# Kernel optimization log

Hardware: AMD Instinct MI355X
Metric: run time of the kernel (lower is better)

The kernel has to match this reference:

```python
import jax, jax.numpy as jnp
import numpy as np


def setup_inputs() -> dict:
    key = jax.random.key(0)
    ks = jax.random.split(key, 6)
    B, S, D_IN, D_OUT, E, R = 4, 2048, 4096, 4096, 8, 16
    x = jax.random.normal(ks[0], (B, S, D_IN), dtype=jnp.float32)
    probs = jax.random.uniform(ks[1], (B, E), dtype=jnp.float32)
    router_probs = probs / jnp.sum(probs, axis=-1, keepdims=True)
    weight = jax.random.normal(ks[2], (D_OUT, D_IN), dtype=jnp.float32) * 0.02
    bias = jax.random.normal(ks[3], (D_OUT,), dtype=jnp.float32) * 0.02
    lora_A = jax.random.normal(ks[4], (E, R, D_IN), dtype=jnp.float32) * 0.02
    lora_B = jax.random.normal(ks[5], (E, D_OUT, R), dtype=jnp.float32) * 0.02
    return {"x": x, "router_probs": router_probs, "weight": weight,
            "bias": bias, "lora_A": lora_A, "lora_B": lora_B}


def reference(x, router_probs, weight, bias, lora_A, lora_B):
    scaling = 2.0
    # base linear: [b,s,i] @ [o,i]^T + bias
    base_out = jnp.einsum('bsi,oi->bso', x, weight) + bias
    # low-rank per-expert projection: [b,s,e,r] (small: r=16)
    mid = jnp.einsum('bsi,eri->bser', x, lora_A)
    # weight by router probs (per batch, per expert) before up-projection
    mid_w = mid * router_probs[:, None, :, None]
    # sum over experts fused into the up-projection contraction
    delta = jnp.einsum('bser,eor->bso', mid_w, lora_B) * scaling
    return base_out + delta
```

## Files before the change

kernel.cpp:

```cpp
#include <hip/hip_runtime.h>


typedef _Float16 half8 __attribute__((ext_vector_type(8)));
typedef _Float16 half4 __attribute__((ext_vector_type(4)));
typedef float    f32x4 __attribute__((ext_vector_type(4)));

#define M_TOT 8192
#define N_TOT 4096
#define K_IN  4096
#define KA    4224
#define NT    132

__device__ __forceinline__ void cvt_store4(_Float16* p, float4 f) {
  half4 h;
  h[0] = (_Float16)f.x; h[1] = (_Float16)f.y;
  h[2] = (_Float16)f.z; h[3] = (_Float16)f.w;
  *(half4*)p = h;
}

template <int LOG2C, int DCOLS>
__global__ __launch_bounds__(256) void convert_f32_f16_t(
    const float* __restrict__ src, _Float16* __restrict__ dst, int total8) {
  for (int i = blockIdx.x * 256 + threadIdx.x; i < total8;
       i += gridDim.x * 256) {
    int base = i << 3;
    int r = base >> LOG2C;
    int c = base & ((1 << LOG2C) - 1);
    const float4* s = (const float4*)(src + (size_t)base);
    float4 f0 = s[0], f1 = s[1];
    half8 h;
    h[0]=(_Float16)f0.x; h[1]=(_Float16)f0.y; h[2]=(_Float16)f0.z; h[3]=(_Float16)f0.w;
    h[4]=(_Float16)f1.x; h[5]=(_Float16)f1.y; h[6]=(_Float16)f1.z; h[7]=(_Float16)f1.w;
    *(half8*)(dst + (size_t)r * DCOLS + c) = h;
  }
}

__global__ __launch_bounds__(256) void wtail_gather_f16(
    const float* __restrict__ loraB, _Float16* __restrict__ Wa) {
  int idx = blockIdx.x * 256 + threadIdx.x;
  int n = idx >> 7, j = idx & 127;
  int e = j >> 4, r = j & 15;
  Wa[(size_t)n * KA + K_IN + j] =
      (_Float16)loraB[((size_t)e * N_TOT + n) * 16 + r];
}

__global__ __launch_bounds__(256) void lorabf_gather_f32(
    const float* __restrict__ loraB, float* __restrict__ lorabf) {
  int idx = blockIdx.x * 256 + threadIdx.x;
  int n = idx >> 7, j = idx & 127;
  int e = j >> 4, r = j & 15;
  lorabf[(size_t)n * 128 + j] = loraB[((size_t)e * N_TOT + n) * 16 + r];
}

__global__ __launch_bounds__(256) void mid2_kernel(
    _Float16* __restrict__ Xa, const _Float16* __restrict__ lAh,
    const float* __restrict__ router) {
  __shared__ _Float16 As[32 * 64];
  __shared__ _Float16 Bs[128 * 64];
  int tid = threadIdx.x, lane = tid & 63, w = tid >> 6;
  int m0 = blockIdx.x * 32;
  int b = m0 >> 11;
  f32x4 acc[2][2] = {};

  int scol = ((lane & 7) ^ (lane >> 3)) * 16;
  int ln15 = lane & 15, ln4 = lane >> 4;

  for (int ks = 0; ks < 64; ++ks) {
    int kb = ks * 128;
    {
      const char* s = (const char*)Xa +
          (size_t)(m0 + w * 8 + (lane >> 3)) * (KA * 2) + kb + scol;
      __builtin_amdgcn_global_load_lds(
          (const __attribute__((address_space(1))) void*)s,
          (__attribute__((address_space(3))) void*)((char*)As + w * 1024 + lane * 16), 16, 0, 0);
    }
#pragma unroll
    for (int i = 0; i < 4; ++i) {
      const char* s = (const char*)lAh +
          (size_t)((w * 4 + i) * 8 + (lane >> 3)) * (4096 * 2) + kb + scol;
      __builtin_amdgcn_global_load_lds(
          (const __attribute__((address_space(1))) void*)s,
          (__attribute__((address_space(3))) void*)((char*)Bs + (w * 4 + i) * 1024 + lane * 16), 16, 0, 0);
    }
    __syncthreads();
#pragma unroll
    for (int kk = 0; kk < 2; ++kk) {
      int rs = (((kk * 4 + ln4) ^ (ln15 & 7)) << 4);
      half8 a[2], bf[2];
#pragma unroll
      for (int mi = 0; mi < 2; ++mi)
        a[mi] = *(const half8*)((const char*)As + (mi * 16 + ln15) * 128 + rs);
#pragma unroll
      for (int ni = 0; ni < 2; ++ni)
        bf[ni] = *(const half8*)((const char*)Bs + (w * 32 + ni * 16 + ln15) * 128 + rs);
#pragma unroll
      for (int mi = 0; mi < 2; ++mi)
#pragma unroll
        for (int ni = 0; ni < 2; ++ni)
          acc[mi][ni] = __builtin_amdgcn_mfma_f32_16x16x32_f16(a[mi], bf[ni], acc[mi][ni], 0, 0, 0);
    }
    __syncthreads();
  }

#pragma unroll
  for (int ni = 0; ni < 2; ++ni) {
    int j = w * 32 + ni * 16 + ln15;
    int e = j >> 4;
    float sc = 2.0f * router[b * 8 + e];
#pragma unroll
    for (int mi = 0; mi < 2; ++mi) {
      f32x4 v = acc[mi][ni];
#pragma unroll
      for (int jj = 0; jj < 4; ++jj) {
        int m = m0 + mi * 16 + ln4 * 4 + jj;
        Xa[(size_t)m * KA + K_IN + j] = (_Float16)(v[jj] * sc);
      }
    }
  }
}

__global__ __launch_bounds__(256) void mid_kernel(
    const float* __restrict__ x, const float* __restrict__ loraA,
    const float* __restrict__ router, float* __restrict__ midw) {
  __shared__ _Float16 As[32 * 64];
  __shared__ _Float16 Bs[128 * 64];
  int tid = threadIdx.x, lane = tid & 63, w = tid >> 6;
  int m0 = blockIdx.x * 32;
  int b = m0 >> 11;
  f32x4 acc[2][2] = {};
  for (int ks = 0; ks < 64; ++ks) {
    int k0 = ks * 64;
#pragma unroll
    for (int it = 0; it < 2; ++it) {
      int idx = tid + it * 256;
      int r = idx >> 4, c4 = idx & 15;
      float4 f = *(const float4*)(x + (size_t)(m0 + r) * K_IN + k0 + c4 * 4);
      cvt_store4(As + r * 64 + c4 * 4, f);
    }
#pragma unroll
    for (int it = 0; it < 8; ++it) {
      int idx = tid + it * 256;
      int r = idx >> 4, c4 = idx & 15;
      float4 f = *(const float4*)(loraA + (size_t)r * K_IN + k0 + c4 * 4);
      cvt_store4(Bs + r * 64 + c4 * 4, f);
    }
    __syncthreads();
#pragma unroll
    for (int kk = 0; kk < 2; ++kk) {
      half8 a[2], bf[2];
#pragma unroll
      for (int mi = 0; mi < 2; ++mi)
        a[mi] = *(const half8*)(As + (mi * 16 + (lane & 15)) * 64 + kk * 32 + (lane >> 4) * 8);
#pragma unroll
      for (int ni = 0; ni < 2; ++ni)
        bf[ni] = *(const half8*)(Bs + (w * 32 + ni * 16 + (lane & 15)) * 64 + kk * 32 + (lane >> 4) * 8);
#pragma unroll
      for (int mi = 0; mi < 2; ++mi)
#pragma unroll
        for (int ni = 0; ni < 2; ++ni)
          acc[mi][ni] = __builtin_amdgcn_mfma_f32_16x16x32_f16(a[mi], bf[ni], acc[mi][ni], 0, 0, 0);
    }
    __syncthreads();
  }
#pragma unroll
  for (int ni = 0; ni < 2; ++ni) {
    int j = w * 32 + ni * 16 + (lane & 15);
    int e = j >> 4;
    float sc = 2.0f * router[b * 8 + e];
#pragma unroll
    for (int mi = 0; mi < 2; ++mi) {
      f32x4 v = acc[mi][ni];
#pragma unroll
      for (int jj = 0; jj < 4; ++jj) {
        int m = m0 + mi * 16 + (lane >> 4) * 4 + jj;
        midw[(size_t)m * 128 + j] = v[jj] * sc;
      }
    }
  }
}

#define BAR    __builtin_amdgcn_s_barrier()
#define SCHED0 __builtin_amdgcn_sched_barrier(0)
#define VMW8   asm volatile("s_waitcnt vmcnt(8)" ::: "memory")
#define VMW4   asm volatile("s_waitcnt vmcnt(4)" ::: "memory")
#define VMW0   asm volatile("s_waitcnt vmcnt(0)" ::: "memory")
#define GLOAD(src, dst) __builtin_amdgcn_global_load_lds( \
    (const __attribute__((address_space(1))) void*)(src), \
    (__attribute__((address_space(3))) void*)(dst), 16, 0, 0)

#define READS(SL) do { \
  _Pragma("unroll") for (int ni = 0; ni < 4; ++ni) \
    bF[ni] = *(const half8*)(LDS + 65536 + (SL) * 16384 + \
                             (wn + ni * 16 + ln15) * 64 + rslot); \
  _Pragma("unroll") for (int mi = 0; mi < 8; ++mi) \
    aF[mi] = *(const half8*)(LDS + (SL) * 16384 + \
                             (wm + mi * 16 + ln15) * 64 + rslot); \
  } while (0)

#define STAGE4(TT, SL) do { \
  const char* sA_ = XpC + (size_t)(TT) * 64; \
  const char* sB_ = WpC + (size_t)(TT) * 64; \
  GLOAD(sA_ + goff0, LDS + (SL) * 16384 + l0); \
  GLOAD(sA_ + goff1, LDS + (SL) * 16384 + l1); \
  GLOAD(sB_ + goff0, LDS + 65536 + (SL) * 16384 + l0); \
  GLOAD(sB_ + goff1, LDS + 65536 + (SL) * 16384 + l1); \
  } while (0)

#define MFMA32 do { \
  _Pragma("unroll") for (int mi = 0; mi < 8; ++mi) \
    _Pragma("unroll") for (int ni = 0; ni < 4; ++ni) \
      acc[mi][ni] = __builtin_amdgcn_mfma_f32_16x16x32_f16( \
          aF[mi], bF[ni], acc[mi][ni], 0, 0, 0); \
  } while (0)

#define TILE_FULL(SL) do { \
  READS(SL); \
  STAGE4(t4 + (SL) + 3, ((SL) + 3) & 3); \
  MFMA32; VMW8; BAR; SCHED0; \
  } while (0)

__global__ __launch_bounds__(512, 2) void gemm256(
    const _Float16* __restrict__ Xa, const _Float16* __restrict__ Wa,
    const float* __restrict__ bias, float* __restrict__ out) {
  __shared__ __align__(16) char LDS[131072];

  int tid = threadIdx.x, lane = tid & 63, w = tid >> 6;
  int ln15 = lane & 15, ln4 = lane >> 4;
  int wm = (w >> 2) * 128, wn = (w & 3) * 64;

  int bid = blockIdx.x;
  int xcd = bid & 7, idx = bid >> 3;
  int mt = (xcd & 3) * 8 + (idx & 7);
  int nt = (xcd >> 2) * 8 + (idx >> 3);
  int m0 = mt << 8, n0 = nt << 8;

  const char* XpC = (const char*)Xa + (size_t)m0 * (KA * 2);
  const char* WpC = (const char*)Wa + (size_t)n0 * (KA * 2);

  int i0 = tid, i1 = tid + 512;
  int goff0 = (i0 >> 2) * (KA * 2) + (((i0 & 3) ^ ((i0 >> 3) & 3)) * 16);
  int goff1 = (i1 >> 2) * (KA * 2) + (((i1 & 3) ^ ((i1 >> 3) & 3)) * 16);
  int l0 = i0 * 16, l1 = i1 * 16;

  int rslot = ((ln4 ^ ((lane >> 1) & 3)) * 16);

  f32x4 acc[8][4] = {};
  half8 aF[8], bF[4];

  STAGE4(0, 0); STAGE4(1, 1); STAGE4(2, 2);
  VMW8; BAR; SCHED0;

#pragma unroll 1
  for (int t4 = 0; t4 < NT - 4; t4 += 4) {
    TILE_FULL(0); TILE_FULL(1); TILE_FULL(2); TILE_FULL(3);
  }

  { READS(0); STAGE4(131, 3); MFMA32; VMW8; BAR; SCHED0; }
  { READS(1); MFMA32; VMW4; BAR; SCHED0; }
  { READS(2); MFMA32; VMW0; BAR; SCHED0; }
  { READS(3); MFMA32; }

#pragma unroll
  for (int ni = 0; ni < 4; ++ni) {
    int n = n0 + wn + ni * 16 + ln15;
    float bz = bias[n];
#pragma unroll
    for (int mi = 0; mi < 8; ++mi) {
      f32x4 v = acc[mi][ni];
      int mb = m0 + wm + mi * 16 + ln4 * 4;
#pragma unroll
      for (int jj = 0; jj < 4; ++jj)
        out[(size_t)(mb + jj) * N_TOT + n] = v[jj] + bz;
    }
  }
}

__global__ __launch_bounds__(256) void gemm_fallback(
    const float* __restrict__ x, const float* __restrict__ wgt,
    const float* __restrict__ midw, const float* __restrict__ lorabf,
    const float* __restrict__ bias, float* __restrict__ out) {
  __shared__ _Float16 As[128 * 64];
  __shared__ _Float16 Bs[128 * 64];
  int tid = threadIdx.x, lane = tid & 63, w = tid >> 6;
  int mt = blockIdx.x & 63, nt = blockIdx.x >> 6;
  int m0 = mt << 7, n0 = nt << 7;
  int wm = (w >> 1) * 64, wn = (w & 1) * 64;
  f32x4 acc[4][4] = {};
  for (int ks = 0; ks < 66; ++ks) {
    int k0 = ks * 64;
    const float *asrc, *bsrc; size_t astr, bstr; int ac, bc;
    if (ks < 64) { asrc = x;    astr = K_IN; ac = k0;        bsrc = wgt;    bstr = K_IN; bc = k0; }
    else         { asrc = midw; astr = 128;  ac = k0 - K_IN; bsrc = lorabf; bstr = 128;  bc = k0 - K_IN; }
#pragma unroll
    for (int it = 0; it < 8; ++it) {
      int idx = tid + it * 256;
      int r = idx >> 4, c4 = idx & 15;
      float4 fa = *(const float4*)(asrc + (size_t)(m0 + r) * astr + ac + c4 * 4);
      cvt_store4(As + r * 64 + c4 * 4, fa);
      float4 fb = *(const float4*)(bsrc + (size_t)(n0 + r) * bstr + bc + c4 * 4);
      cvt_store4(Bs + r * 64 + c4 * 4, fb);
    }
    __syncthreads();
#pragma unroll
    for (int kk = 0; kk < 2; ++kk) {
      half8 a[4], bf[4];
#pragma unroll
      for (int mi = 0; mi < 4; ++mi)
        a[mi] = *(const half8*)(As + (wm + mi * 16 + (lane & 15)) * 64 + kk * 32 + (lane >> 4) * 8);
#pragma unroll
      for (int ni = 0; ni < 4; ++ni)
        bf[ni] = *(const half8*)(Bs + (wn + ni * 16 + (lane & 15)) * 64 + kk * 32 + (lane >> 4) * 8);
#pragma unroll
      for (int mi = 0; mi < 4; ++mi)
#pragma unroll
        for (int ni = 0; ni < 4; ++ni)
          acc[mi][ni] = __builtin_amdgcn_mfma_f32_16x16x32_f16(a[mi], bf[ni], acc[mi][ni], 0, 0, 0);
    }
    __syncthreads();
  }
#pragma unroll
  for (int ni = 0; ni < 4; ++ni) {
    int n = n0 + wn + ni * 16 + (lane & 15);
    float bz = bias[n];
#pragma unroll
    for (int mi = 0; mi < 4; ++mi) {
      f32x4 v = acc[mi][ni];
      int mbase = m0 + wm + mi * 16 + (lane >> 4) * 4;
#pragma unroll
      for (int jj = 0; jj < 4; ++jj)
        out[(size_t)(mbase + jj) * N_TOT + n] = v[jj] + bz;
    }
  }
}

extern "C" void kernel_launch(void* const* d_in, const int* in_sizes, int n_in,
                              void* d_out, int out_size, void* d_ws, size_t ws_size,
                              hipStream_t stream) {
  const float* x      = (const float*)d_in[0];
  const float* router = (const float*)d_in[1];
  const float* wgt    = (const float*)d_in[2];
  const float* bias   = (const float*)d_in[3];
  const float* loraA  = (const float*)d_in[4];
  const float* loraB  = (const float*)d_in[5];
  float* out = (float*)d_out;
  char* ws = (char*)d_ws;

  const size_t XAUG_B = (size_t)M_TOT * KA * 2;
  const size_t WAUG_B = (size_t)N_TOT * KA * 2;
  const size_t LAH_B  = (size_t)128 * K_IN * 2;
  const size_t MIDW_B = (size_t)M_TOT * 128 * 4;
  bool fast = ws_size >= XAUG_B + WAUG_B + LAH_B;

  if (fast) {
    _Float16* Xa  = (_Float16*)ws;
    _Float16* Wa  = (_Float16*)(ws + XAUG_B);
    _Float16* lAh = (_Float16*)(ws + XAUG_B + WAUG_B);
    convert_f32_f16_t<12, KA><<<2048, 256, 0, stream>>>(x,   Xa, M_TOT * K_IN / 8);
    convert_f32_f16_t<12, KA><<<2048, 256, 0, stream>>>(wgt, Wa, N_TOT * K_IN / 8);
    convert_f32_f16_t<12, 4096><<<256, 256, 0, stream>>>(loraA, lAh, 128 * K_IN / 8);
    wtail_gather_f16<<<2048, 256, 0, stream>>>(loraB, Wa);
    mid2_kernel<<<256, 256, 0, stream>>>(Xa, lAh, router);
    gemm256<<<512, 512, 0, stream>>>(Xa, Wa, bias, out);
  } else {
    float* midw   = (float*)ws;
    float* lorabf = (float*)(ws + MIDW_B);
    lorabf_gather_f32<<<2048, 256, 0, stream>>>(loraB, lorabf);
    mid_kernel<<<256, 256, 0, stream>>>(x, loraA, router, midw);
    gemm_fallback<<<2048, 256, 0, stream>>>(x, wgt, midw, lorabf, bias, out);
  }
}
```

Measured before the change: 364.8 us.

## Switch main GEMM to 32x32 MFMA and split-K the LoRA down-projection

The main GEMM switches from 16x16x32 to 32x32x16 MFMA tiles. The shared-memory layout changes so each 64-lane fragment is read contiguously, replacing the XOR swizzle. The LoRA mid projection moves from a 256-block serial-K kernel to a 2048-block split-K kernel that reads fp32 x directly and accumulates with atomics into a zeroed fp32 buffer. A separate pass then scales by the router and packs into the augmented X. This adds extra launches, atomics and a reread of x in fp32 in exchange for more parallelism and a different GEMM inner loop.

Measured after the change: 472.3 us. 1.29x slower.

```diff
diff --git a/kernel.cpp b/kernel.cpp
--- a/kernel.cpp
+++ b/kernel.cpp
@@ -3,7 +3,8 @@
 
 typedef _Float16 half8 __attribute__((ext_vector_type(8)));
 typedef _Float16 half4 __attribute__((ext_vector_type(4)));
-typedef float    f32x4 __attribute__((ext_vector_type(4)));
+typedef float    f32x4  __attribute__((ext_vector_type(4)));
+typedef float    f32x16 __attribute__((ext_vector_type(16)));
 
 #define M_TOT 8192
 #define N_TOT 4096
@@ -52,6 +53,78 @@
   lorabf[(size_t)n * 128 + j] = loraB[((size_t)e * N_TOT + n) * 16 + r];
 }
 
+__global__ __launch_bounds__(256) void zero_f4(float4* p, int n) {
+  int i = blockIdx.x * 256 + threadIdx.x;
+  if (i < n) { float4 z = {0.f, 0.f, 0.f, 0.f}; p[i] = z; }
+}
+
+__global__ __launch_bounds__(256) void midk_kernel(
+    const float* __restrict__ x, const float* __restrict__ loraA,
+    float* __restrict__ midw) {
+  __shared__ _Float16 As[32 * 64];
+  __shared__ _Float16 Bs[128 * 64];
+  int tid = threadIdx.x, lane = tid & 63, w = tid >> 6;
+  int m0 = (blockIdx.x >> 3) * 32;
+  int ks0 = (blockIdx.x & 7) * 8;
+  f32x4 acc[2][2] = {};
+  for (int ks = ks0; ks < ks0 + 8; ++ks) {
+    int k0 = ks * 64;
+#pragma unroll
+    for (int it = 0; it < 2; ++it) {
+      int idx = tid + it * 256;
+      int r = idx >> 4, c4 = idx & 15;
+      float4 f = *(const float4*)(x + (size_t)(m0 + r) * K_IN + k0 + c4 * 4);
+      cvt_store4(As + r * 64 + c4 * 4, f);
+    }
+#pragma unroll
+    for (int it = 0; it < 8; ++it) {
+      int idx = tid + it * 256;
+      int r = idx >> 4, c4 = idx & 15;
+      float4 f = *(const float4*)(loraA + (size_t)r * K_IN + k0 + c4 * 4);
+      cvt_store4(Bs + r * 64 + c4 * 4, f);
+    }
+    __syncthreads();
+#pragma unroll
+    for (int kk = 0; kk < 2; ++kk) {
+      half8 a[2], bf[2];
+#pragma unroll
+      for (int mi = 0; mi < 2; ++mi)
+        a[mi] = *(const half8*)(As + (mi * 16 + (lane & 15)) * 64 + kk * 32 + (lane >> 4) * 8);
+#pragma unroll
+      for (int ni = 0; ni < 2; ++ni)
+        bf[ni] = *(const half8*)(Bs + (w * 32 + ni * 16 + (lane & 15)) * 64 + kk * 32 + (lane >> 4) * 8);
+#pragma unroll
+      for (int mi = 0; mi < 2; ++mi)
+#pragma unroll
+        for (int ni = 0; ni < 2; ++ni)
+          acc[mi][ni] = __builtin_amdgcn_mfma_f32_16x16x32_f16(a[mi], bf[ni], acc[mi][ni], 0, 0, 0);
+    }
+    __syncthreads();
+  }
+#pragma unroll
+  for (int ni = 0; ni < 2; ++ni) {
+    int j = w * 32 + ni * 16 + (lane & 15);
+#pragma unroll
+    for (int mi = 0; mi < 2; ++mi) {
+      f32x4 v = acc[mi][ni];
+#pragma unroll
+      for (int jj = 0; jj < 4; ++jj) {
+        int m = m0 + mi * 16 + (lane >> 4) * 4 + jj;
+        atomicAdd(&midw[(size_t)m * 128 + j], v[jj]);
+      }
+    }
+  }
+}
+
+__global__ __launch_bounds__(256) void scale_pack(
+    const float* __restrict__ midw, const float* __restrict__ router,
+    _Float16* __restrict__ Xa) {
+  int idx = blockIdx.x * 256 + threadIdx.x;
+  int m = idx >> 7, j = idx & 127;
+  int b = m >> 11, e = j >> 4;
+  Xa[(size_t)m * KA + K_IN + j] = (_Float16)(2.0f * router[b * 8 + e] * midw[idx]);
+}
+
 __global__ __launch_bounds__(256) void mid2_kernel(
     _Float16* __restrict__ Xa, const _Float16* __restrict__ lAh,
     const float* __restrict__ router) {
@@ -61,10 +134,8 @@
   int m0 = blockIdx.x * 32;
   int b = m0 >> 11;
   f32x4 acc[2][2] = {};
-
   int scol = ((lane & 7) ^ (lane >> 3)) * 16;
   int ln15 = lane & 15, ln4 = lane >> 4;
-
   for (int ks = 0; ks < 64; ++ks) {
     int kb = ks * 128;
     {
@@ -101,7 +172,6 @@
     }
     __syncthreads();
   }
-
 #pragma unroll
   for (int ni = 0; ni < 2; ++ni) {
     int j = w * 32 + ni * 16 + ln15;
@@ -189,34 +259,37 @@
     (__attribute__((address_space(3))) void*)(dst), 16, 0, 0)
 
 #define READS(SL) do { \
-  _Pragma("unroll") for (int ni = 0; ni < 4; ++ni) \
-    bF[ni] = *(const half8*)(LDS + 65536 + (SL) * 16384 + \
-                             (wn + ni * 16 + ln15) * 64 + rslot); \
-  _Pragma("unroll") for (int mi = 0; mi < 8; ++mi) \
-    aF[mi] = *(const half8*)(LDS + (SL) * 16384 + \
-                             (wm + mi * 16 + ln15) * 64 + rslot); \
+  _Pragma("unroll") for (int ni = 0; ni < 2; ++ni) \
+    _Pragma("unroll") for (int kk = 0; kk < 2; ++kk) \
+      bF[ni][kk] = *(const half8*)(LDS + 65536 + (SL) * 16384 + \
+                                   (((nbB + ni) * 2 + kk) << 10) + lane * 16); \
+  _Pragma("unroll") for (int mi = 0; mi < 4; ++mi) \
+    _Pragma("unroll") for (int kk = 0; kk < 2; ++kk) \
+      aF[mi][kk] = *(const half8*)(LDS + (SL) * 16384 + \
+                                   (((mbB + mi) * 2 + kk) << 10) + lane * 16); \
   } while (0)
 
 #define STAGE4(TT, SL) do { \
   const char* sA_ = XpC + (size_t)(TT) * 64; \
   const char* sB_ = WpC + (size_t)(TT) * 64; \
-  GLOAD(sA_ + goff0, LDS + (SL) * 16384 + l0); \
-  GLOAD(sA_ + goff1, LDS + (SL) * 16384 + l1); \
-  GLOAD(sB_ + goff0, LDS + 65536 + (SL) * 16384 + l0); \
-  GLOAD(sB_ + goff1, LDS + 65536 + (SL) * 16384 + l1); \
+  GLOAD(sA_ + goffA[0], LDS + (SL) * 16384 + lof[0]); \
+  GLOAD(sA_ + goffA[1], LDS + (SL) * 16384 + lof[1]); \
+  GLOAD(sB_ + goffA[0], LDS + 65536 + (SL) * 16384 + lof[0]); \
+  GLOAD(sB_ + goffA[1], LDS + 65536 + (SL) * 16384 + lof[1]); \
   } while (0)
 
-#define MFMA32 do { \
-  _Pragma("unroll") for (int mi = 0; mi < 8; ++mi) \
-    _Pragma("unroll") for (int ni = 0; ni < 4; ++ni) \
-      acc[mi][ni] = __builtin_amdgcn_mfma_f32_16x16x32_f16( \
-          aF[mi], bF[ni], acc[mi][ni], 0, 0, 0); \
+#define MFMA16X do { \
+  _Pragma("unroll") for (int mi = 0; mi < 4; ++mi) \
+    _Pragma("unroll") for (int ni = 0; ni < 2; ++ni) \
+      _Pragma("unroll") for (int kk = 0; kk < 2; ++kk) \
+        acc[mi][ni] = __builtin_amdgcn_mfma_f32_32x32x16_f16( \
+            aF[mi][kk], bF[ni][kk], acc[mi][ni], 0, 0, 0); \
   } while (0)
 
 #define TILE_FULL(SL) do { \
   READS(SL); \
   STAGE4(t4 + (SL) + 3, ((SL) + 3) & 3); \
-  MFMA32; VMW8; BAR; SCHED0; \
+  MFMA16X; VMW8; BAR; SCHED0; \
   } while (0)
 
 __global__ __launch_bounds__(512, 2) void gemm256(
@@ -225,8 +298,8 @@
   __shared__ __align__(16) char LDS[131072];
 
   int tid = threadIdx.x, lane = tid & 63, w = tid >> 6;
-  int ln15 = lane & 15, ln4 = lane >> 4;
-  int wm = (w >> 2) * 128, wn = (w & 3) * 64;
+  int mbB = (w >> 2) * 4;
+  int nbB = (w & 3) * 2;
 
   int bid = blockIdx.x;
   int xcd = bid & 7, idx = bid >> 3;
@@ -237,15 +310,19 @@
   const char* XpC = (const char*)Xa + (size_t)m0 * (KA * 2);
   const char* WpC = (const char*)Wa + (size_t)n0 * (KA * 2);
 
-  int i0 = tid, i1 = tid + 512;
-  int goff0 = (i0 >> 2) * (KA * 2) + (((i0 & 3) ^ ((i0 >> 3) & 3)) * 16);
-  int goff1 = (i1 >> 2) * (KA * 2) + (((i1 & 3) ^ ((i1 >> 3) & 3)) * 16);
-  int l0 = i0 * 16, l1 = i1 * 16;
-
-  int rslot = ((ln4 ^ ((lane >> 1) & 3)) * 16);
-
-  f32x4 acc[8][4] = {};
-  half8 aF[8], bF[4];
+  int goffA[2], lof[2];
+#pragma unroll
+  for (int j = 0; j < 2; ++j) {
+    int ix = j * 512 + tid;
+    int c = ix >> 6, lp = ix & 63;
+    int row = (c >> 1) * 32 + (lp & 31);
+    int kb = ((c & 1) << 5) + ((lp >> 5) << 4);
+    goffA[j] = row * (KA * 2) + kb;
+    lof[j] = ix * 16;
+  }
+
+  f32x16 acc[4][2] = {};
+  half8 aF[4][2], bF[2][2];
 
   STAGE4(0, 0); STAGE4(1, 1); STAGE4(2, 2);
   VMW8; BAR; SCHED0;
@@ -255,22 +332,24 @@
     TILE_FULL(0); TILE_FULL(1); TILE_FULL(2); TILE_FULL(3);
   }
 
-  { READS(0); STAGE4(131, 3); MFMA32; VMW8; BAR; SCHED0; }
-  { READS(1); MFMA32; VMW4; BAR; SCHED0; }
-  { READS(2); MFMA32; VMW0; BAR; SCHED0; }
-  { READS(3); MFMA32; }
-
-#pragma unroll
-  for (int ni = 0; ni < 4; ++ni) {
-    int n = n0 + wn + ni * 16 + ln15;
+  { READS(0); STAGE4(131, 3); MFMA16X; VMW8; BAR; SCHED0; }
+  { READS(1); MFMA16X; VMW4; BAR; SCHED0; }
+  { READS(2); MFMA16X; VMW0; BAR; SCHED0; }
+  { READS(3); MFMA16X; }
+
+#pragma unroll
+  for (int ni = 0; ni < 2; ++ni) {
+    int n = n0 + (nbB + ni) * 32 + (lane & 31);
     float bz = bias[n];
 #pragma unroll
-    for (int mi = 0; mi < 8; ++mi) {
-      f32x4 v = acc[mi][ni];
-      int mb = m0 + wm + mi * 16 + ln4 * 4;
-#pragma unroll
-      for (int jj = 0; jj < 4; ++jj)
-        out[(size_t)(mb + jj) * N_TOT + n] = v[jj] + bz;
+    for (int mi = 0; mi < 4; ++mi) {
+      f32x16 v = acc[mi][ni];
+      int rb = m0 + (mbB + mi) * 32 + ((lane >> 5) << 2);
+#pragma unroll
+      for (int reg = 0; reg < 16; ++reg) {
+        int r = rb + (reg & 3) + ((reg >> 2) << 3);
+        out[(size_t)r * N_TOT + n] = v[reg] + bz;
+      }
     }
   }
 }
@@ -349,9 +428,20 @@
   const size_t WAUG_B = (size_t)N_TOT * KA * 2;
   const size_t LAH_B  = (size_t)128 * K_IN * 2;
   const size_t MIDW_B = (size_t)M_TOT * 128 * 4;
-  bool fast = ws_size >= XAUG_B + WAUG_B + LAH_B;
-
-  if (fast) {
+  const size_t MIDF_B = MIDW_B;
+
+  if (ws_size >= XAUG_B + WAUG_B + MIDW_B) {
+    _Float16* Xa  = (_Float16*)ws;
+    _Float16* Wa  = (_Float16*)(ws + XAUG_B);
+    float* midw   = (float*)(ws + XAUG_B + WAUG_B);
+    convert_f32_f16_t<12, KA><<<2048, 256, 0, stream>>>(x,   Xa, M_TOT * K_IN / 8);
+    convert_f32_f16_t<12, KA><<<2048, 256, 0, stream>>>(wgt, Wa, N_TOT * K_IN / 8);
+    wtail_gather_f16<<<2048, 256, 0, stream>>>(loraB, Wa);
+    zero_f4<<<1024, 256, 0, stream>>>((float4*)midw, M_TOT * 128 / 4);
+    midk_kernel<<<2048, 256, 0, stream>>>(x, loraA, midw);
+    scale_pack<<<4096, 256, 0, stream>>>(midw, router, Xa);
+    gemm256<<<512, 512, 0, stream>>>(Xa, Wa, bias, out);
+  } else if (ws_size >= XAUG_B + WAUG_B + LAH_B) {
     _Float16* Xa  = (_Float16*)ws;
     _Float16* Wa  = (_Float16*)(ws + XAUG_B);
     _Float16* lAh = (_Float16*)(ws + XAUG_B + WAUG_B);
@@ -363,7 +453,7 @@
     gemm256<<<512, 512, 0, stream>>>(Xa, Wa, bias, out);
   } else {
     float* midw   = (float*)ws;
-    float* lorabf = (float*)(ws + MIDW_B);
+    float* lorabf = (float*)(ws + MIDF_B);
     lorabf_gather_f32<<<2048, 256, 0, stream>>>(loraB, lorabf);
     mid_kernel<<<256, 256, 0, stream>>>(x, loraA, router, midw);
     gemm_fallback<<<2048, 256, 0, stream>>>(x, wgt, midw, lorabf, bias, out);
```
